# Performance work log

Hardware: AMD Instinct MI355X
Metric: run time of the kernel (lower is better)

The kernel has to match this reference:

```python
import jax, jax.numpy as jnp
import numpy as np

TAU = 2.0      # LIF time constant
EPS = 1e-5     # BatchNorm eps
ALPHA = 4.0    # sigmoid surrogate-gradient sharpness (spikingjelly default)

@jax.custom_vjp
def _spike(x):
    return (x >= 0.0).astype(x.dtype)

def _spike_fwd(x):
    return _spike(x), x

def _spike_bwd(x, g):
    s = jax.nn.sigmoid(ALPHA * x)
    return (g * ALPHA * s * (1.0 - s),)

_spike.defvjp(_spike_fwd, _spike_bwd)

def lif(x_seq, v_th=1.0):
    # Multi-step LIF with hard reset to 0, detach_reset=True, v[0]=0.
    # x_seq: (T, ...) ; scan over T.
    def step(v, x):
        v = v + (x - v) / TAU
        s = _spike(v - v_th)
        v = v * (1.0 - jax.lax.stop_gradient(s))  # detach_reset
        return v, s
    _, s_seq = jax.lax.scan(step, jnp.zeros_like(x_seq[0]), x_seq)
    return s_seq

def bn(x, gamma, beta, mean, var):
    # inference-mode BatchNorm2d on (T,B,C,H,W), params (C,)
    sh = (1, 1, -1, 1, 1)
    scale = gamma.reshape(sh) * jax.lax.rsqrt(var.reshape(sh) + EPS)
    return (x - mean.reshape(sh)) * scale + beta.reshape(sh)

def conv1x1(x, w):
    # 1x1 conv == channel matmul; x: (T,B,C,H,W), w: (Cout,Cin)
    return jnp.einsum('tbchw,dc->tbdhw', x, w)

def setup_inputs() -> dict:
    key = jax.random.key(0)
    ks = jax.random.split(key, 24)
    T, B, C, H, W = 4, 32, 384, 16, 16
    d = {}
    d['x'] = jax.random.normal(ks[0], (T, B, C, H, W), jnp.float32)
    for i, p in enumerate(['q', 'k', 'v']):
        base = 1 + 5 * i
        d[p + '_w'] = jax.random.normal(ks[base], (C, C), jnp.float32) * 0.05
        d[p + '_gamma'] = jax.random.uniform(ks[base + 1], (C,), jnp.float32) + 0.5
        d[p + '_beta'] = jax.random.normal(ks[base + 2], (C,), jnp.float32) * 0.1
        d[p + '_mean'] = jax.random.normal(ks[base + 3], (C,), jnp.float32) * 0.1
        d[p + '_var'] = jax.random.uniform(ks[base + 4], (C,), jnp.float32) + 0.5
    d['proj_w'] = jax.random.normal(ks[16], (C, C), jnp.float32) * 0.05
    d['proj_b'] = jax.random.normal(ks[17], (C,), jnp.float32) * 0.1
    d['proj_gamma'] = jax.random.uniform(ks[18], (C,), jnp.float32) + 0.5
    d['proj_beta'] = jax.random.normal(ks[19], (C,), jnp.float32) * 0.1
    d['proj_mean'] = jax.random.normal(ks[20], (C,), jnp.float32) * 0.1
    d['proj_var'] = jax.random.uniform(ks[21], (C,), jnp.float32) + 0.5
    d['num_heads'] = 8
    return d

def reference(x, q_w, q_gamma, q_beta, q_mean, q_var,
              k_w, k_gamma, k_beta, k_mean, k_var,
              v_w, v_gamma, v_beta, v_mean, v_var,
              proj_w, proj_b, proj_gamma, proj_beta, proj_mean, proj_var,
              num_heads):
    T, B, C, H, W = x.shape
    N = H * W
    Ch = C // num_heads
    identity = x
    xs = lif(x)  # shortcut_lif

    def branch(w, g, b, m, var_):
        o = lif(bn(conv1x1(xs, w), g, b, m, var_))  # (T,B,C,H,W), binary spikes
        # flatten(3).transpose(-1,-2).reshape(T,B,N,h,Ch).permute -> (T,B,h,N,Ch)
        return o.reshape(T, B, num_heads, Ch, N).transpose(0, 1, 2, 4, 3)

    q = branch(q_w, q_gamma, q_beta, q_mean, q_var)
    k = branch(k_w, k_gamma, k_beta, k_mean, k_var)
    v = branch(v_w, v_gamma, v_beta, v_mean, v_var)

    kv = (k * v).sum(axis=3, keepdims=True)      # (T,B,h,1,Ch) linear-attn reduce over N
    kv = lif(kv, v_th=0.5)                       # talking_heads_lif
    y = q * kv                                   # (T,B,h,N,Ch)
    y = y.transpose(0, 1, 2, 4, 3).reshape(T, B, C, H, W)
    y = conv1x1(y, proj_w) + proj_b.reshape(1, 1, -1, 1, 1)
    y = bn(y, proj_gamma, proj_beta, proj_mean, proj_var)
    return (y + identity, v)
```

## Files before the change

kernel.cpp:

```cpp
#include <hip/hip_runtime.h>

typedef unsigned short u16;
typedef unsigned char u8;
typedef signed char i8;
typedef int i32x4 __attribute__((ext_vector_type(4)));
typedef int i32x16 __attribute__((ext_vector_type(16)));
typedef float f32x4 __attribute__((ext_vector_type(4)));
typedef u16 u16x8 __attribute__((ext_vector_type(8)));
typedef u8 u8x16 __attribute__((ext_vector_type(16)));

__device__ __forceinline__ void gload16(const void* g, void* l) {
    __builtin_amdgcn_global_load_lds(
        (const __attribute__((address_space(1))) void*)g,
        (__attribute__((address_space(3))) void*)l, 16, 0, 0);
}

__global__ __launch_bounds__(256) void prep(const float* __restrict__ X, u8* __restrict__ Xt,
    const float* __restrict__ qw, const float* __restrict__ kw,
    const float* __restrict__ vw, const float* __restrict__ pw,
    i8* __restrict__ Wq, float* __restrict__ Sc, float* __restrict__ KVraw) {
    const int bid = blockIdx.x;
    if (bid < 768) {
        __shared__ __attribute__((aligned(16))) u8 s2[4][32][136];
        const int c0 = (bid % 3) * 128;
        const int n0 = ((bid / 3) & 7) * 32;
        const int b = bid / 24;
        const int n_l = threadIdx.x & 31, cg = threadIdx.x >> 5;
        for (int jj = 0; jj < 16; jj++) {
            int c_l = cg + jj * 8;
            float vm = 0.f;
            #pragma unroll
            for (int t = 0; t < 4; t++) {
                float xv = X[(((long)t * 32 + b) * 384 + c0 + c_l) * 256 + n0 + n_l];
                vm += (xv - vm) * 0.5f;
                u8 sp = 0;
                if (vm >= 1.0f) { sp = 1; vm = 0.f; }
                s2[t][n_l][c_l] = sp;
            }
        }
        __syncthreads();
        const int c16 = (threadIdx.x & 7) << 4;
        const int n = (threadIdx.x >> 3) & 31;
        #pragma unroll
        for (int t = 0; t < 4; t++) {
            u8x16 v = *(const u8x16*)&s2[t][n][c16];
            *(u8x16*)&Xt[(((long)b * 256 + n0 + n) * 4 + t) * 384 + c0 + c16] = v;
        }
    } else {
        const int wv = bid - 768;
        const int w = threadIdx.x >> 6, lane = threadIdx.x & 63;
        const int r = wv * 4 + w;
        const int m = r / 384, d = r - m * 384;
        const float* srcs[4] = {qw, kw, vw, pw};
        const float* row = srcs[m] + (long)d * 384;
        float a[6]; float mx = 0.f;
        #pragma unroll
        for (int jj = 0; jj < 6; jj++) { a[jj] = row[lane + (jj << 6)]; mx = fmaxf(mx, fabsf(a[jj])); }
        #pragma unroll
        for (int off = 1; off < 64; off <<= 1) mx = fmaxf(mx, __shfl_xor(mx, off));
        float scale = mx * (1.f / 127.f);
        float sinv = mx > 0.f ? 127.f / mx : 0.f;
        if (lane == 0) Sc[r] = scale;
        i8* dst0 = Wq + (long)(m == 3 ? 9 : m * 3) * 147456 + (long)d * 384;
        #pragma unroll
        for (int jj = 0; jj < 6; jj++) {
            float x = a[jj] * sinv;
            float q1 = rintf(x);         float r1 = x - q1;
            float q2 = rintf(r1 * 128.f); float r2 = r1 * 128.f - q2;
            float q3 = rintf(r2 * 128.f);
            int c = lane + (jj << 6);
            dst0[c] = (i8)(int)q1;
            dst0[147456 + c] = (i8)(int)q2;
            if (m != 3) dst0[2 * 147456 + c] = (i8)(int)q3;
        }
        const int idx = wv * 256 + threadIdx.x;
        if (idx < 49152) KVraw[idx] = 0.f;
    }
}

template<int NL>
__device__ __forceinline__ void gemm_i8(const u8* __restrict__ A, const i8* __restrict__ B,
                                        long lstride, char* lds8, int m0, int n0, i32x16 (&acc)[NL][2]) {
    const int tid = threadIdx.x, l = tid & 63, w = tid >> 6;
    const int wm = (w & 1) << 6, wn = (w >> 1) << 5;
    const int col = l & 31, kg = l >> 5;
    const int rA = tid >> 2, sl = tid & 3;
    const int cs = (sl ^ ((rA >> 1) & 3)) << 4;
    const u8* Ap = A + (long)(m0 + rA) * 384 + cs;
    const i8* Bp = B + (long)(n0 + rA) * 384 + cs;
    char* dst = lds8 + tid * 16;
    for (int kk = 0; kk < 384; kk += 64) {
        gload16(Ap + kk, dst);
        gload16(Ap + 24576 + kk, dst + 4096);
        #pragma unroll
        for (int p = 0; p < NL; p++)
            gload16(Bp + p * lstride + kk, dst + 8192 + p * 4096);
        __syncthreads();
        #pragma unroll
        for (int c = 0; c < 2; c++) {
            i32x4 af[2];
            #pragma unroll
            for (int i = 0; i < 2; i++) {
                int ra = wm + (i << 5) + col;
                int sa = ((2 * c + kg) ^ ((ra >> 1) & 3)) << 4;
                af[i] = *(const i32x4*)(lds8 + ra * 64 + sa);
            }
            int rb = wn + col;
            int sb = ((2 * c + kg) ^ ((rb >> 1) & 3)) << 4;
            #pragma unroll
            for (int p = 0; p < NL; p++) {
                i32x4 bf = *(const i32x4*)(lds8 + 8192 + p * 4096 + rb * 64 + sb);
                #pragma unroll
                for (int i = 0; i < 2; i++)
                    acc[p][i] = __builtin_amdgcn_mfma_i32_32x32x32_i8(af[i], bf, acc[p][i], 0, 0, 0);
            }
        }
        __syncthreads();
    }
}

__global__ __launch_bounds__(256, 4) void k2(
    const u8* __restrict__ Xt, const i8* __restrict__ Wq, const float* __restrict__ Sc,
    const float* __restrict__ g0, const float* __restrict__ b0, const float* __restrict__ m0_, const float* __restrict__ v0_,
    const float* __restrict__ g1, const float* __restrict__ b1, const float* __restrict__ m1_, const float* __restrict__ v1_,
    const float* __restrict__ g2, const float* __restrict__ b2, const float* __restrict__ m2_, const float* __restrict__ v2_,
    u8* __restrict__ oq, u8* __restrict__ ok, u8* __restrict__ ov, float* __restrict__ out1)
{
    __shared__ __attribute__((aligned(16))) char lds8[20480];
    const int bid = blockIdx.x;
    const int xcd = bid & 7, bi = bid >> 3;
    const int mt = (bi / 18) * 8 + xcd;
    const int sub = bi % 18;
    const int m0 = mt * 128, d0 = (sub % 6) * 64, br = sub / 6;
    const float* G  = br == 0 ? g0  : (br == 1 ? g1  : g2);
    const float* Be = br == 0 ? b0  : (br == 1 ? b1  : b2);
    const float* Mu = br == 0 ? m0_ : (br == 1 ? m1_ : m2_);
    const float* Va = br == 0 ? v0_ : (br == 1 ? v1_ : v2_);

    i32x16 acc[3][2];
    #pragma unroll
    for (int p = 0; p < 3; p++)
        #pragma unroll
        for (int i = 0; i < 2; i++)
            #pragma unroll
            for (int r = 0; r < 16; r++) acc[p][i][r] = 0;
    gemm_i8<3>(Xt, Wq + (long)br * 3 * 147456, 147456L, lds8, m0, d0, acc);

    const int tid = threadIdx.x, l = tid & 63, w = tid >> 6;
    const int wm = (w & 1) << 6, wn = (w >> 1) << 5;
    const int col = l & 31;
    const int d = d0 + wn + col;
    const float scb = G[d] / sqrtf(Va[d] + 1e-5f);
    const float mu = Mu[d], be = Be[d];
    const float wsc = Sc[br * 384 + d];
    u8* tile8 = (u8*)lds8;
    const float c1 = 0.0078125f, c2 = 6.103515625e-05f;
    #pragma unroll
    for (int i = 0; i < 2; i++)
        #pragma unroll
        for (int q = 0; q < 4; q++) {
            float vm = 0.f;
            int mb = wm + (i << 5) + (q << 3) + ((l >> 5) << 2);
            #pragma unroll
            for (int t = 0; t < 4; t++) {
                int reg = q * 4 + t;
                float f = (float)acc[0][i][reg] + (float)acc[1][i][reg] * c1
                        + (float)acc[2][i][reg] * c2;
                float bn = (f * wsc - mu) * scb + be;
                vm += (bn - vm) * 0.5f;
                u8 s = 0;
                if (vm >= 1.0f) { s = 1; vm = 0.f; }
                tile8[(mb + t) * 80 + wn + col] = s;
            }
        }
    __syncthreads();
    const int ml = tid >> 1, cb = (tid & 1) << 5;
    u8* Out8 = br == 0 ? oq : (br == 1 ? ok : ov);
    uint4 w0 = *(const uint4*)&tile8[ml * 80 + cb];
    uint4 w1 = *(const uint4*)&tile8[ml * 80 + cb + 16];
    *(uint4*)&Out8[(long)(m0 + ml) * 384 + d0 + cb] = w0;
    *(uint4*)&Out8[(long)(m0 + ml) * 384 + d0 + cb + 16] = w1;
    if (br == 2) {
        const int b = m0 >> 10, n_base = (m0 >> 2) & 255;
        const int dl = tid & 63, d2 = d0 + dl;
        const int h = d2 / 48, ch = d2 % 48;
        for (int q = 0; q < 32; q++) {
            int mlq = (tid >> 6) + (q << 2);
            int t = mlq & 3, n = n_base + (mlq >> 2);
            out1[((((long)t * 32 + b) * 8 + h) * 256 + n) * 48 + ch] =
                tile8[mlq * 80 + dl] ? 1.0f : 0.f;
        }
    }
}

__global__ __launch_bounds__(384) void k3a(const u8* __restrict__ Ks, const u8* __restrict__ Vs,
                                           float* __restrict__ kv_raw) {
    const int b = blockIdx.y, nc = blockIdx.x;
    const int d4 = threadIdx.x * 4, t = threadIdx.y;
    int cnt0 = 0, cnt1 = 0, cnt2 = 0, cnt3 = 0;
    for (int nl = 0; nl < 32; nl++) {
        const long row = ((long)b * 256 + nc * 32 + nl) * 4 + t;
        uchar4 kk = *(const uchar4*)&Ks[row * 384 + d4];
        uchar4 vv = *(const uchar4*)&Vs[row * 384 + d4];
        cnt0 += (kk.x & vv.x); cnt1 += (kk.y & vv.y);
        cnt2 += (kk.z & vv.z); cnt3 += (kk.w & vv.w);
    }
    float* dst = &kv_raw[((long)t * 32 + b) * 384 + d4];
    atomicAdd(dst + 0, (float)cnt0);
    atomicAdd(dst + 1, (float)cnt1);
    atomicAdd(dst + 2, (float)cnt2);
    atomicAdd(dst + 3, (float)cnt3);
}

__global__ __launch_bounds__(384) void k3b(const float* __restrict__ kv_raw, u8* __restrict__ kvs) {
    const int b = blockIdx.x, d = threadIdx.x;
    float vm = 0.f;
    #pragma unroll
    for (int t = 0; t < 4; t++) {
        vm += (kv_raw[((long)t * 32 + b) * 384 + d] - vm) * 0.5f;
        u8 sp = 0;
        if (vm >= 0.5f) { sp = 1; vm = 0.f; }
        kvs[((long)t * 32 + b) * 384 + d] = sp;
    }
}

__global__ __launch_bounds__(256) void k3c(const u8* __restrict__ Qs, const u8* __restrict__ KVs,
                                           u8* __restrict__ Y) {
    const long i16 = ((long)blockIdx.x * 256 + threadIdx.x) * 16;
    const int m = (int)(i16 / 384), d16 = (int)(i16 % 384);
    const int t = m & 3, b = m >> 10;
    uint4 q = *(const uint4*)(Qs + i16);
    uint4 kvv = *(const uint4*)(KVs + ((long)(t * 32 + b) * 384 + d16));
    uint4 y;
    y.x = q.x & kvv.x; y.y = q.y & kvv.y; y.z = q.z & kvv.z; y.w = q.w & kvv.w;
    *(uint4*)(Y + i16) = y;
}

__global__ __launch_bounds__(256, 4) void k4(
    const u8* __restrict__ Y, const i8* __restrict__ Pq, const float* __restrict__ Scp,
    const float* __restrict__ PB, const float* __restrict__ PG, const float* __restrict__ PBe,
    const float* __restrict__ PM, const float* __restrict__ PV,
    const float* __restrict__ X, float* __restrict__ O)
{
    __shared__ __attribute__((aligned(16))) char lds8[33792];
    const int bid = blockIdx.x;
    const int xcd = bid & 7, bi = bid >> 3;
    const int mt = (bi / 6) * 8 + xcd;
    const int m0 = mt * 128, e0 = (bi % 6) * 64;
    i32x16 acc[2][2];
    #pragma unroll
    for (int p = 0; p < 2; p++)
        #pragma unroll
        for (int i = 0; i < 2; i++)
            #pragma unroll
            for (int r = 0; r < 16; r++) acc[p][i][r] = 0;
    gemm_i8<2>(Y, Pq, 147456L, lds8, m0, e0, acc);

    const int tid = threadIdx.x, l = tid & 63, w = tid >> 6;
    const int wm = (w & 1) << 6, wn = (w >> 1) << 5;
    const int col = l & 31;
    const int e = e0 + wn + col;
    const float scb = PG[e] / sqrtf(PV[e] + 1e-5f);
    const float mu = PM[e], be = PBe[e], pbb = PB[e];
    const float wsc = Scp[e];
    float* smemf = (float*)lds8;
    const float c1 = 0.0078125f;
    #pragma unroll
    for (int i = 0; i < 2; i++)
        #pragma unroll
        for (int q = 0; q < 4; q++)
            #pragma unroll
            for (int t = 0; t < 4; t++) {
                int reg = q * 4 + t;
                float f = (float)acc[0][i][reg] + (float)acc[1][i][reg] * c1;
                float z = (f * wsc + pbb - mu) * scb + be;
                int m = wm + (i << 5) + (q << 3) + ((l >> 5) << 2) + t;
                smemf[(wn + col) * 132 + m] = z;
            }
    __syncthreads();
    const int b = m0 >> 10, n_base = (m0 >> 2) & 255;
    const int n_l = tid & 31;
    #pragma unroll
    for (int ei = 0; ei < 8; ei++) {
        int e_l = (tid >> 5) + (ei << 3);
        f32x4 v = *(const f32x4*)&smemf[e_l * 132 + (n_l << 2)];
        #pragma unroll
        for (int t = 0; t < 4; t++) {
            long gi = (((long)t * 32 + b) * 384 + e0 + e_l) * 256 + n_base + n_l;
            O[gi] = v[t] + X[gi];
        }
    }
}

extern "C" void kernel_launch(void* const* d_in, const int* in_sizes, int n_in,
                              void* d_out, int out_size, void* d_ws, size_t ws_size,
                              hipStream_t stream) {
    (void)in_sizes; (void)n_in; (void)out_size; (void)ws_size;
    const float* x   = (const float*)d_in[0];
    const float* qw  = (const float*)d_in[1];
    const float* qg  = (const float*)d_in[2];
    const float* qb  = (const float*)d_in[3];
    const float* qm  = (const float*)d_in[4];
    const float* qv  = (const float*)d_in[5];
    const float* kw  = (const float*)d_in[6];
    const float* kg  = (const float*)d_in[7];
    const float* kb  = (const float*)d_in[8];
    const float* km  = (const float*)d_in[9];
    const float* kv  = (const float*)d_in[10];
    const float* vw  = (const float*)d_in[11];
    const float* vg  = (const float*)d_in[12];
    const float* vb  = (const float*)d_in[13];
    const float* vm  = (const float*)d_in[14];
    const float* vv  = (const float*)d_in[15];
    const float* pw  = (const float*)d_in[16];
    const float* pb  = (const float*)d_in[17];
    const float* pg  = (const float*)d_in[18];
    const float* pbe = (const float*)d_in[19];
    const float* pm  = (const float*)d_in[20];
    const float* pv  = (const float*)d_in[21];

    float* out0 = (float*)d_out;
    float* out1 = out0 + 12582912;
    char*  ob   = (char*)d_out;
    u8*    Qs8  = (u8*)ob;
    u8*    Xt8  = (u8*)(ob + 12582912);
    char*  ws   = (char*)d_ws;
    u8*    Ks8  = (u8*)ws;
    u8*    Vs8  = (u8*)ws + 12582912;
    u8*    Yb8  = (u8*)ws;
    float* KVraw = (float*)(ws + 25165824);
    u8*    KVs8  = (u8*)(ws + 25362432);
    i8*    Wq    = (i8*)(ws + 25411584);
    float* Sc    = (float*)(ws + 27033600);

    hipLaunchKernelGGL(prep, dim3(1152), dim3(256), 0, stream, x, Xt8, qw, kw, vw, pw, Wq, Sc, KVraw);
    hipLaunchKernelGGL(k2, dim3(4608), dim3(256), 0, stream,
                       Xt8, Wq, Sc,
                       qg, qb, qm, qv,
                       kg, kb, km, kv,
                       vg, vb, vm, vv,
                       Qs8, Ks8, Vs8, out1);
    hipLaunchKernelGGL(k3a, dim3(8, 32), dim3(96, 4), 0, stream, Ks8, Vs8, KVraw);
    hipLaunchKernelGGL(k3b, dim3(32), dim3(384), 0, stream, KVraw, KVs8);
    hipLaunchKernelGGL(k3c, dim3(3072), dim3(256), 0, stream, Qs8, KVs8, Yb8);
    hipLaunchKernelGGL(k4, dim3(768 * 2), dim3(256), 0, stream,
                       Yb8, Wq + 9 * 147456L, Sc + 3 * 384, pb, pg, pbe, pm, pv, x, out0);
}
```

Baseline: 286.9 us.

## Chunk int8 operands into 64-wide K blocks and use nontemporal loads/stores

Stores spike activations, the quantized weights and the branch outputs in a K-chunked layout (6 chunks of 64 channels, each chunk contiguous over rows), so every GEMM K-step reads one contiguous 64-byte row slice per row. The kv-reduce, masking and projection kernels are updated to index the new layout. Streaming reads of X and writes of outputs now use nontemporal hints, and the v-output writeback is vectorized to float4 stores. This is meant to improve coalescing and cache behaviour of the tile loads and the output traffic. The cost is more complex indexing and a larger stride between K chunks.

```diff
diff --git a/kernel.cpp b/kernel.cpp
--- a/kernel.cpp
+++ b/kernel.cpp
@@ -6,8 +6,10 @@
 typedef int i32x4 __attribute__((ext_vector_type(4)));
 typedef int i32x16 __attribute__((ext_vector_type(16)));
 typedef float f32x4 __attribute__((ext_vector_type(4)));
-typedef u16 u16x8 __attribute__((ext_vector_type(8)));
+typedef unsigned u32x4 __attribute__((ext_vector_type(4)));
 typedef u8 u8x16 __attribute__((ext_vector_type(16)));
+
+#define CHS 2097152L
 
 __device__ __forceinline__ void gload16(const void* g, void* l) {
     __builtin_amdgcn_global_load_lds(
@@ -31,7 +33,7 @@
             float vm = 0.f;
             #pragma unroll
             for (int t = 0; t < 4; t++) {
-                float xv = X[(((long)t * 32 + b) * 384 + c0 + c_l) * 256 + n0 + n_l];
+                float xv = __builtin_nontemporal_load(&X[(((long)t * 32 + b) * 384 + c0 + c_l) * 256 + n0 + n_l]);
                 vm += (xv - vm) * 0.5f;
                 u8 sp = 0;
                 if (vm >= 1.0f) { sp = 1; vm = 0.f; }
@@ -41,10 +43,12 @@
         __syncthreads();
         const int c16 = (threadIdx.x & 7) << 4;
         const int n = (threadIdx.x >> 3) & 31;
+        const int cglob = c0 + c16;
+        const int ch = cglob >> 6, off = cglob & 63;
         #pragma unroll
         for (int t = 0; t < 4; t++) {
             u8x16 v = *(const u8x16*)&s2[t][n][c16];
-            *(u8x16*)&Xt[(((long)b * 256 + n0 + n) * 4 + t) * 384 + c0 + c16] = v;
+            *(u8x16*)&Xt[(long)ch * CHS + ((long)(b * 256 + n0 + n) * 4 + t) * 64 + off] = v;
         }
     } else {
         const int wv = bid - 768;
@@ -61,17 +65,17 @@
         float scale = mx * (1.f / 127.f);
         float sinv = mx > 0.f ? 127.f / mx : 0.f;
         if (lane == 0) Sc[r] = scale;
-        i8* dst0 = Wq + (long)(m == 3 ? 9 : m * 3) * 147456 + (long)d * 384;
+        i8* dstb = Wq + (long)(m == 3 ? 9 : m * 3) * 147456 + (long)d * 64;
         #pragma unroll
         for (int jj = 0; jj < 6; jj++) {
             float x = a[jj] * sinv;
             float q1 = rintf(x);         float r1 = x - q1;
             float q2 = rintf(r1 * 128.f); float r2 = r1 * 128.f - q2;
             float q3 = rintf(r2 * 128.f);
-            int c = lane + (jj << 6);
-            dst0[c] = (i8)(int)q1;
-            dst0[147456 + c] = (i8)(int)q2;
-            if (m != 3) dst0[2 * 147456 + c] = (i8)(int)q3;
+            int co = jj * 24576 + lane;
+            dstb[co] = (i8)(int)q1;
+            dstb[147456 + co] = (i8)(int)q2;
+            if (m != 3) dstb[2 * 147456 + co] = (i8)(int)q3;
         }
         const int idx = wv * 256 + threadIdx.x;
         if (idx < 49152) KVraw[idx] = 0.f;
@@ -80,21 +84,21 @@
 
 template<int NL>
 __device__ __forceinline__ void gemm_i8(const u8* __restrict__ A, const i8* __restrict__ B,
-                                        long lstride, char* lds8, int m0, int n0, i32x16 (&acc)[NL][2]) {
+                                        char* lds8, int m0, int n0, i32x16 (&acc)[NL][2]) {
     const int tid = threadIdx.x, l = tid & 63, w = tid >> 6;
     const int wm = (w & 1) << 6, wn = (w >> 1) << 5;
     const int col = l & 31, kg = l >> 5;
     const int rA = tid >> 2, sl = tid & 3;
     const int cs = (sl ^ ((rA >> 1) & 3)) << 4;
-    const u8* Ap = A + (long)(m0 + rA) * 384 + cs;
-    const i8* Bp = B + (long)(n0 + rA) * 384 + cs;
+    const u8* Ap = A + (long)(m0 + rA) * 64 + cs;
+    const i8* Bp = B + (long)(n0 + rA) * 64 + cs;
     char* dst = lds8 + tid * 16;
-    for (int kk = 0; kk < 384; kk += 64) {
-        gload16(Ap + kk, dst);
-        gload16(Ap + 24576 + kk, dst + 4096);
+    for (int ck = 0; ck < 6; ck++) {
+        gload16(Ap + ck * CHS, dst);
+        gload16(Ap + ck * CHS + 4096, dst + 4096);
         #pragma unroll
         for (int p = 0; p < NL; p++)
-            gload16(Bp + p * lstride + kk, dst + 8192 + p * 4096);
+            gload16(Bp + p * 147456 + ck * 24576, dst + 8192 + p * 4096);
         __syncthreads();
         #pragma unroll
         for (int c = 0; c < 2; c++) {
@@ -144,7 +148,7 @@
         for (int i = 0; i < 2; i++)
             #pragma unroll
             for (int r = 0; r < 16; r++) acc[p][i][r] = 0;
-    gemm_i8<3>(Xt, Wq + (long)br * 3 * 147456, 147456L, lds8, m0, d0, acc);
+    gemm_i8<3>(Xt, Wq + (long)br * 3 * 147456, lds8, m0, d0, acc);
 
     const int tid = threadIdx.x, l = tid & 63, w = tid >> 6;
     const int wm = (w & 1) << 6, wn = (w >> 1) << 5;
@@ -176,19 +180,25 @@
     __syncthreads();
     const int ml = tid >> 1, cb = (tid & 1) << 5;
     u8* Out8 = br == 0 ? oq : (br == 1 ? ok : ov);
-    uint4 w0 = *(const uint4*)&tile8[ml * 80 + cb];
-    uint4 w1 = *(const uint4*)&tile8[ml * 80 + cb + 16];
-    *(uint4*)&Out8[(long)(m0 + ml) * 384 + d0 + cb] = w0;
-    *(uint4*)&Out8[(long)(m0 + ml) * 384 + d0 + cb + 16] = w1;
+    long obase = (long)(d0 >> 6) * CHS + (long)(m0 + ml) * 64 + cb;
+    u32x4 w0 = *(const u32x4*)&tile8[ml * 80 + cb];
+    u32x4 w1 = *(const u32x4*)&tile8[ml * 80 + cb + 16];
+    __builtin_nontemporal_store(w0, (u32x4*)(Out8 + obase));
+    __builtin_nontemporal_store(w1, (u32x4*)(Out8 + obase + 16));
     if (br == 2) {
         const int b = m0 >> 10, n_base = (m0 >> 2) & 255;
-        const int dl = tid & 63, d2 = d0 + dl;
-        const int h = d2 / 48, ch = d2 % 48;
-        for (int q = 0; q < 32; q++) {
-            int mlq = (tid >> 6) + (q << 2);
+        const int dl4 = (tid & 15) << 2;
+        const int d2 = d0 + dl4;
+        const int h = d2 / 48, chn = d2 - h * 48;
+        #pragma unroll
+        for (int q = 0; q < 8; q++) {
+            int mlq = (tid >> 4) + (q << 4);
             int t = mlq & 3, n = n_base + (mlq >> 2);
-            out1[((((long)t * 32 + b) * 8 + h) * 256 + n) * 48 + ch] =
-                tile8[mlq * 80 + dl] ? 1.0f : 0.f;
+            f32x4 v;
+            #pragma unroll
+            for (int r = 0; r < 4; r++) v[r] = tile8[mlq * 80 + dl4 + r] ? 1.0f : 0.f;
+            long gi = ((((long)t * 32 + b) * 8 + h) * 256 + n) * 48 + chn;
+            __builtin_nontemporal_store(v, (f32x4*)&out1[gi]);
         }
     }
 }
@@ -197,11 +207,12 @@
                                            float* __restrict__ kv_raw) {
     const int b = blockIdx.y, nc = blockIdx.x;
     const int d4 = threadIdx.x * 4, t = threadIdx.y;
+    const long cbase = (long)(d4 >> 6) * CHS + (d4 & 63);
     int cnt0 = 0, cnt1 = 0, cnt2 = 0, cnt3 = 0;
     for (int nl = 0; nl < 32; nl++) {
         const long row = ((long)b * 256 + nc * 32 + nl) * 4 + t;
-        uchar4 kk = *(const uchar4*)&Ks[row * 384 + d4];
-        uchar4 vv = *(const uchar4*)&Vs[row * 384 + d4];
+        uchar4 kk = *(const uchar4*)&Ks[cbase + row * 64];
+        uchar4 vv = *(const uchar4*)&Vs[cbase + row * 64];
         cnt0 += (kk.x & vv.x); cnt1 += (kk.y & vv.y);
         cnt2 += (kk.z & vv.z); cnt3 += (kk.w & vv.w);
     }
@@ -226,14 +237,16 @@
 
 __global__ __launch_bounds__(256) void k3c(const u8* __restrict__ Qs, const u8* __restrict__ KVs,
                                            u8* __restrict__ Y) {
-    const long i16 = ((long)blockIdx.x * 256 + threadIdx.x) * 16;
-    const int m = (int)(i16 / 384), d16 = (int)(i16 % 384);
+    const int u = blockIdx.x * 256 + threadIdx.x;
+    const int off16 = (u & 3) << 4;
+    const int m = (u >> 2) & 32767;
+    const int ch = u >> 17;
     const int t = m & 3, b = m >> 10;
-    uint4 q = *(const uint4*)(Qs + i16);
-    uint4 kvv = *(const uint4*)(KVs + ((long)(t * 32 + b) * 384 + d16));
-    uint4 y;
-    y.x = q.x & kvv.x; y.y = q.y & kvv.y; y.z = q.z & kvv.z; y.w = q.w & kvv.w;
-    *(uint4*)(Y + i16) = y;
+    const long ca = (long)ch * CHS + (long)m * 64 + off16;
+    u32x4 q = __builtin_nontemporal_load((const u32x4*)(Qs + ca));
+    u32x4 kvv = *(const u32x4*)(KVs + ((long)(t * 32 + b) * 384 + ch * 64 + off16));
+    u32x4 y = q & kvv;
+    __builtin_nontemporal_store(y, (u32x4*)(Y + ca));
 }
 
 __global__ __launch_bounds__(256, 4) void k4(
@@ -254,7 +267,7 @@
         for (int i = 0; i < 2; i++)
             #pragma unroll
             for (int r = 0; r < 16; r++) acc[p][i][r] = 0;
-    gemm_i8<2>(Y, Pq, 147456L, lds8, m0, e0, acc);
+    gemm_i8<2>(Y, Pq, lds8, m0, e0, acc);
 
     const int tid = threadIdx.x, l = tid & 63, w = tid >> 6;
     const int wm = (w & 1) << 6, wn = (w >> 1) << 5;
@@ -287,7 +300,8 @@
         #pragma unroll
         for (int t = 0; t < 4; t++) {
             long gi = (((long)t * 32 + b) * 384 + e0 + e_l) * 256 + n_base + n_l;
-            O[gi] = v[t] + X[gi];
+            float xv = __builtin_nontemporal_load(&X[gi]);
+            __builtin_nontemporal_store(v[t] + xv, &O[gi]);
         }
     }
 }
```

Result: no change. 286.0 us (-0.3%).
